# Kernel tuning notes

Hardware: AMD Instinct MI355X
Metric: run time of the kernel (lower is better)

Reference implementation:

```python
import jax, jax.numpy as jnp
import numpy as np

N = 1024
IN_F = 128
H0 = 192  # num_features * 2
H1 = 96   # num_features * 1
BN_EPS = 1e-5
SLOPE = 0.01  # LeakyReLU default negative slope


def setup_inputs() -> dict:
    key = jax.random.key(0)
    ks = jax.random.split(key, 8)
    node_feat = jax.random.normal(ks[0], (N, IN_F), dtype=jnp.float32)
    W0 = jax.random.normal(ks[1], (H0, IN_F), dtype=jnp.float32) * 0.05
    g0 = jnp.ones((H0,), jnp.float32); b0 = jnp.zeros((H0,), jnp.float32)
    m0 = jnp.zeros((H0,), jnp.float32); v0 = jnp.ones((H0,), jnp.float32)
    W1 = jax.random.normal(ks[2], (H1, H0), dtype=jnp.float32) * 0.05
    g1 = jnp.ones((H1,), jnp.float32); b1 = jnp.zeros((H1,), jnp.float32)
    m1 = jnp.zeros((H1,), jnp.float32); v1 = jnp.ones((H1,), jnp.float32)
    Wout = jax.random.normal(ks[3], (1, H1), dtype=jnp.float32) * 0.05
    bout = jnp.zeros((1,), jnp.float32)
    return dict(node_feat=node_feat, W0=W0, g0=g0, b0=b0, m0=m0, v0=v0,
                W1=W1, g1=g1, b1=b1, m1=m1, v1=v1, Wout=Wout, bout=bout)


def _bn(x, g, b, m, v):
    # BatchNorm2d in eval mode over channel axis (last axis here)
    return (x - m) * (g * jax.lax.rsqrt(v + BN_EPS)) + b


def _leaky(x):
    return jnp.where(x >= 0, x, SLOPE * x)


def reference(node_feat, W0, g0, b0, m0, v0, W1, g1, b1, m1, v1, Wout, bout):
    n = node_feat.shape[0]
    # pairwise abs diff: [N, N, F] (symmetric, so torch's i/j transpose is a no-op)
    x_ij = jnp.abs(node_feat[:, None, :] - node_feat[None, :, :])
    # 1x1 convs == per-(i,j) matmuls over channel axis
    h = _leaky(_bn(jnp.einsum('ijf,cf->ijc', x_ij, W0), g0, b0, m0, v0))
    h = _leaky(_bn(jnp.einsum('ijc,dc->ijd', h, W1), g1, b1, m1, v1))
    logits = jnp.einsum('ijd,od->ijo', h, Wout)[..., 0] + bout[0]  # [N, N]
    sim_val = jax.nn.sigmoid(logits)
    edge = sim_val + jnp.eye(n, dtype=sim_val.dtype) + 1e-6
    # torch sums over dim=1 of [1, N, N] -> normalize over the row index i
    edge = edge / jnp.sum(edge, axis=0, keepdims=True)
    return edge[None], sim_val  # edge_feat [1, N, N], sim_val [N, N]
```

## Files before the change

kernel.cpp:

```cpp
#include <hip/hip_runtime.h>
#include <hip/hip_bf16.h>
#include <math.h>

typedef float v4f __attribute__((ext_vector_type(4)));
typedef __bf16 bf16x8 __attribute__((ext_vector_type(8)));
typedef __bf16 bf16x4 __attribute__((ext_vector_type(4)));

#define NN   1024
#define INF  128
#define H0C  192
#define H1C  96

#define WS_W0BF   0
#define WS_W1BF   49152
#define WS_BN0SW  86016
#define WS_BN1SW  86784
#define WS_WOUTSW 87168
#define WS_PART   91648

__global__ __launch_bounds__(256) void prep_kernel(
    const float* __restrict__ W0, const float* __restrict__ g0,
    const float* __restrict__ b0, const float* __restrict__ m0,
    const float* __restrict__ v0, const float* __restrict__ W1,
    const float* __restrict__ g1, const float* __restrict__ b1,
    const float* __restrict__ m1, const float* __restrict__ v1,
    const float* __restrict__ Wout, char* __restrict__ ws)
{
    int e = blockIdx.x * 256 + threadIdx.x;
    __bf16* w0bf = (__bf16*)(ws + WS_W0BF);
    __bf16* w1bf = (__bf16*)(ws + WS_W1BF);
    float* bn0sw = (float*)(ws + WS_BN0SW);
    float* bn1sw = (float*)(ws + WS_BN1SW);
    float* woutsw = (float*)(ws + WS_WOUTSW);
    if (e < 24576) {
        int j = e & 7, lane = (e >> 3) & 63, t = e >> 9;
        int ks = t & 3, mt = t >> 2;
        int c = mt * 16 + (lane & 15);
        int k = ks * 32 + ((lane >> 4) << 3) + j;
        float s = g0[c] * rsqrtf(v0[c] + 1e-5f);
        w0bf[e] = (__bf16)(W0[c * INF + k] * s);
    } else if (e < 43008) {
        int e2 = e - 24576;
        int j = e2 & 7, lane = (e2 >> 3) & 63, t = e2 >> 9;
        int ks = t % 6, mt = t / 6;
        int c = mt * 16 + (lane & 15);
        int k = ks * 32 + ((lane >> 4) << 3) + j;
        float s = g1[c] * rsqrtf(v1[c] + 1e-5f);
        w1bf[e2] = (__bf16)(W1[c * H0C + k] * s);
    } else if (e < 43200) {
        int e3 = e - 43008;
        int q = e3 / 48, rem = e3 % 48, cm = rem >> 2, r = rem & 3;
        int c = cm * 16 + q * 4 + r;
        float s = g0[c] * rsqrtf(v0[c] + 1e-5f);
        bn0sw[e3] = b0[c] - m0[c] * s;
    } else if (e < 43296) {
        int e4 = e - 43200;
        int q = e4 / 24, rem = e4 % 24, mt = rem >> 2, r = rem & 3;
        int c = mt * 16 + q * 4 + r;
        float s = g1[c] * rsqrtf(v1[c] + 1e-5f);
        bn1sw[e4] = b1[c] - m1[c] * s;
    } else if (e < 43392) {
        int e5 = e - 43296;
        int q = e5 / 24, rem = e5 % 24, mt = rem >> 2, r = rem & 3;
        woutsw[e5] = Wout[mt * 16 + q * 4 + r];
    }
}

__global__ __launch_bounds__(256, 3) void edgenet_main(
    const float* __restrict__ feat, const char* __restrict__ ws,
    const float* __restrict__ boutp, float* __restrict__ sim_out)
{
    __shared__ __align__(16) char smem[51200];
    const int tid = threadIdx.x;
    const int lane = tid & 63;
    const int wave = tid >> 6;
    const int l16 = lane & 15;
    const int quad = lane >> 4;

    const int id = blockIdx.x;
    int bi = (int)((129.0f - sqrtf(16641.0f - 4.0f * (float)id)) * 0.5f);
    while (bi > 0 && bi * (129 - bi) > id) --bi;
    while ((bi + 1) * (128 - bi) <= id) ++bi;
    const int bj = 2 * bi + (id - bi * (129 - bi));
    const int i0 = bi << 4;
    const int j0 = bj << 3;
    const int jb = j0 + wave * 2;

    #pragma unroll
    for (int it = 0; it < 8; ++it) {
        int c = it * 256 + tid;
        int p = c >> 4;
        int f0 = (c & 15) << 3;
        int ii = p & 15, jj = p >> 4;
        const float* fi = feat + (i0 + ii) * INF + f0;
        const float* fj = feat + (j0 + jj) * INF + f0;
        float4 a0 = *(const float4*)fi;
        float4 a1 = *(const float4*)(fi + 4);
        float4 q0 = *(const float4*)fj;
        float4 q1 = *(const float4*)(fj + 4);
        bf16x8 x;
        x[0] = (__bf16)fabsf(a0.x - q0.x);
        x[1] = (__bf16)fabsf(a0.y - q0.y);
        x[2] = (__bf16)fabsf(a0.z - q0.z);
        x[3] = (__bf16)fabsf(a0.w - q0.w);
        x[4] = (__bf16)fabsf(a1.x - q1.x);
        x[5] = (__bf16)fabsf(a1.y - q1.y);
        x[6] = (__bf16)fabsf(a1.z - q1.z);
        x[7] = (__bf16)fabsf(a1.w - q1.w);
        *(bf16x8*)(smem + p * 272 + f0 * 2) = x;
    }
    __syncthreads();

    const bf16x8* w0v = (const bf16x8*)(ws + WS_W0BF);
    const bf16x8* w1v = (const bf16x8*)(ws + WS_W1BF);
    const float* bn0sw = (const float*)(ws + WS_BN0SW);
    const float* bn1sw = (const float*)(ws + WS_BN1SW);

    v4f acc1[3][8];
    #pragma unroll
    for (int mt = 0; mt < 3; ++mt) {
        v4f bb = *(const v4f*)(bn0sw + (quad * 12 + wave * 3 + mt) * 4);
        #pragma unroll
        for (int nt = 0; nt < 8; ++nt)
            acc1[mt][nt] = bb;
    }
    #pragma unroll
    for (int ks = 0; ks < 4; ++ks) {
        bf16x8 xk[8];
        #pragma unroll
        for (int nt = 0; nt < 8; ++nt)
            xk[nt] = *(const bf16x8*)(smem + (nt * 16 + l16) * 272 + ks * 64 + quad * 16);
        #pragma unroll
        for (int mt = 0; mt < 3; ++mt) {
            bf16x8 w = w0v[((wave * 3 + mt) * 4 + ks) * 64 + lane];
            #pragma unroll
            for (int nt = 0; nt < 8; ++nt)
                acc1[mt][nt] = __builtin_amdgcn_mfma_f32_16x16x32_bf16(
                    w, xk[nt], acc1[mt][nt], 0, 0, 0);
        }
    }
    __syncthreads();

    #pragma unroll
    for (int mt = 0; mt < 3; ++mt) {
        int chb = (wave * 3 + mt) * 16 + quad * 4;
        #pragma unroll
        for (int nt = 0; nt < 8; ++nt) {
            bf16x4 pk;
            #pragma unroll
            for (int r = 0; r < 4; ++r) {
                float v = acc1[mt][nt][r];
                v = fmaxf(v, 0.01f * v);
                pk[r] = (__bf16)v;
            }
            *(bf16x4*)(smem + (nt * 16 + l16) * 400 + chb * 2) = pk;
        }
    }
    __syncthreads();

    v4f acc2[6][2];
    #pragma unroll
    for (int mt = 0; mt < 6; ++mt) {
        v4f bb = *(const v4f*)(bn1sw + (quad * 6 + mt) * 4);
        acc2[mt][0] = bb;
        acc2[mt][1] = bb;
    }
    #pragma unroll
    for (int ks = 0; ks < 6; ++ks) {
        bf16x8 h0, h1;
        h0 = *(const bf16x8*)(smem + ((2 * wave + 0) * 16 + l16) * 400 + ks * 64 + quad * 16);
        h1 = *(const bf16x8*)(smem + ((2 * wave + 1) * 16 + l16) * 400 + ks * 64 + quad * 16);
        #pragma unroll
        for (int mt = 0; mt < 6; ++mt) {
            bf16x8 w = w1v[(mt * 6 + ks) * 64 + lane];
            acc2[mt][0] = __builtin_amdgcn_mfma_f32_16x16x32_bf16(w, h0, acc2[mt][0], 0, 0, 0);
            acc2[mt][1] = __builtin_amdgcn_mfma_f32_16x16x32_bf16(w, h1, acc2[mt][1], 0, 0, 0);
        }
    }

    const float* woutsw = (const float*)(ws + WS_WOUTSW);
    float part[2] = {0.f, 0.f};
    #pragma unroll
    for (int mt = 0; mt < 6; ++mt) {
        v4f wo = *(const v4f*)(woutsw + (quad * 6 + mt) * 4);
        #pragma unroll
        for (int t = 0; t < 2; ++t)
            #pragma unroll
            for (int r = 0; r < 4; ++r) {
                float v = acc2[mt][t][r];
                v = fmaxf(v, 0.01f * v);
                part[t] = fmaf(v, wo[r], part[t]);
            }
    }
    #pragma unroll
    for (int t = 0; t < 2; ++t) {
        part[t] += __shfl_xor(part[t], 16, 64);
        part[t] += __shfl_xor(part[t], 32, 64);
    }
    float z = (quad & 1) ? part[1] : part[0];
    float sv = 1.f / (1.f + expf(-(z + boutp[0])));
    if (quad < 2)
        sim_out[(i0 + l16) * NN + jb + (quad & 1)] = sv;
    else
        sim_out[(jb + (quad & 1)) * NN + i0 + l16] = sv;
}

__global__ __launch_bounds__(256) void colsum_kernel(
    const float* __restrict__ sim, float* __restrict__ part)
{
    __shared__ float red[4][64];
    int jl = threadIdx.x & 63;
    int ig = threadIdx.x >> 6;
    int j = blockIdx.x * 64 + jl;
    int ibase = blockIdx.y * 64 + ig * 16;
    float s = 0.f;
    #pragma unroll
    for (int r = 0; r < 16; ++r)
        s += sim[(ibase + r) * NN + j];
    red[ig][jl] = s;
    __syncthreads();
    if (ig == 0) {
        float t = red[0][jl] + red[1][jl] + red[2][jl] + red[3][jl];
        part[blockIdx.y * NN + j] = t;
    }
}

__global__ __launch_bounds__(256) void edge_kernel(
    const float* __restrict__ partsum, const float* __restrict__ sim,
    float* __restrict__ edge)
{
    int i = blockIdx.x;
    int jc = threadIdx.x << 2;
    float4 t = {0.f, 0.f, 0.f, 0.f};
    #pragma unroll
    for (int p = 0; p < 16; ++p) {
        float4 q = *(const float4*)(partsum + p * NN + jc);
        t.x += q.x; t.y += q.y; t.z += q.z; t.w += q.w;
    }
    const float cadd = 1.0f + (float)NN * 1e-6f;
    float4 s = *(const float4*)(sim + i * NN + jc);
    float4 o;
    o.x = (s.x + (i == jc + 0 ? 1.f : 0.f) + 1e-6f) / (t.x + cadd);
    o.y = (s.y + (i == jc + 1 ? 1.f : 0.f) + 1e-6f) / (t.y + cadd);
    o.z = (s.z + (i == jc + 2 ? 1.f : 0.f) + 1e-6f) / (t.z + cadd);
    o.w = (s.w + (i == jc + 3 ? 1.f : 0.f) + 1e-6f) / (t.w + cadd);
    *(float4*)(edge + i * NN + jc) = o;
}

extern "C" void kernel_launch(void* const* d_in, const int* in_sizes, int n_in,
                              void* d_out, int out_size, void* d_ws, size_t ws_size,
                              hipStream_t stream)
{
    const float* feat = (const float*)d_in[0];
    const float* W0   = (const float*)d_in[1];
    const float* g0   = (const float*)d_in[2];
    const float* b0   = (const float*)d_in[3];
    const float* m0   = (const float*)d_in[4];
    const float* v0   = (const float*)d_in[5];
    const float* W1   = (const float*)d_in[6];
    const float* g1   = (const float*)d_in[7];
    const float* b1   = (const float*)d_in[8];
    const float* m1   = (const float*)d_in[9];
    const float* v1   = (const float*)d_in[10];
    const float* Wout = (const float*)d_in[11];
    const float* bout = (const float*)d_in[12];
    char* ws = (char*)d_ws;
    float* edge = (float*)d_out;
    float* sim  = edge + NN * NN;
    float* part = (float*)(ws + WS_PART);

    prep_kernel<<<dim3(170), dim3(256), 0, stream>>>(
        W0, g0, b0, m0, v0, W1, g1, b1, m1, v1, Wout, ws);
    edgenet_main<<<dim3(4160), dim3(256), 0, stream>>>(feat, ws, bout, sim);
    colsum_kernel<<<dim3(16, 16), dim3(256), 0, stream>>>(sim, part);
    edge_kernel<<<dim3(1024), dim3(256), 0, stream>>>(part, sim, edge);
}
```

Before: 154.1 us.

## Fuse all stages into one persistent cooperative kernel with grid syncs

Replaces the four kernel launches (weight prep, main MLP, column sum, normalization) with a single cooperative persistent kernel that loops over tile ids and separates phases with grid-wide syncs. The column sum now produces reciprocal normalizers directly, so the final pass multiplies instead of divides. The pairwise-diff staging also reuses each i-row's feature loads across the 8 j rows. This removes launch gaps and the partial-sum buffer, at the cost of grid-sync overhead, a grid size capped at 704 persistent blocks, and an occupancy query on every call.

```diff
diff --git a/kernel.cpp b/kernel.cpp
--- a/kernel.cpp
+++ b/kernel.cpp
@@ -1,6 +1,9 @@
 #include <hip/hip_runtime.h>
+#include <hip/hip_cooperative_groups.h>
 #include <hip/hip_bf16.h>
 #include <math.h>
+
+namespace cg = cooperative_groups;
 
 typedef float v4f __attribute__((ext_vector_type(4)));
 typedef __bf16 bf16x8 __attribute__((ext_vector_type(8)));
@@ -16,59 +19,18 @@
 #define WS_BN0SW  86016
 #define WS_BN1SW  86784
 #define WS_WOUTSW 87168
-#define WS_PART   91648
-
-__global__ __launch_bounds__(256) void prep_kernel(
+#define WS_CINV   87552
+
+__global__ __launch_bounds__(256, 3) void edgenet_all(
+    const float* __restrict__ feat,
     const float* __restrict__ W0, const float* __restrict__ g0,
     const float* __restrict__ b0, const float* __restrict__ m0,
     const float* __restrict__ v0, const float* __restrict__ W1,
     const float* __restrict__ g1, const float* __restrict__ b1,
     const float* __restrict__ m1, const float* __restrict__ v1,
-    const float* __restrict__ Wout, char* __restrict__ ws)
-{
-    int e = blockIdx.x * 256 + threadIdx.x;
-    __bf16* w0bf = (__bf16*)(ws + WS_W0BF);
-    __bf16* w1bf = (__bf16*)(ws + WS_W1BF);
-    float* bn0sw = (float*)(ws + WS_BN0SW);
-    float* bn1sw = (float*)(ws + WS_BN1SW);
-    float* woutsw = (float*)(ws + WS_WOUTSW);
-    if (e < 24576) {
-        int j = e & 7, lane = (e >> 3) & 63, t = e >> 9;
-        int ks = t & 3, mt = t >> 2;
-        int c = mt * 16 + (lane & 15);
-        int k = ks * 32 + ((lane >> 4) << 3) + j;
-        float s = g0[c] * rsqrtf(v0[c] + 1e-5f);
-        w0bf[e] = (__bf16)(W0[c * INF + k] * s);
-    } else if (e < 43008) {
-        int e2 = e - 24576;
-        int j = e2 & 7, lane = (e2 >> 3) & 63, t = e2 >> 9;
-        int ks = t % 6, mt = t / 6;
-        int c = mt * 16 + (lane & 15);
-        int k = ks * 32 + ((lane >> 4) << 3) + j;
-        float s = g1[c] * rsqrtf(v1[c] + 1e-5f);
-        w1bf[e2] = (__bf16)(W1[c * H0C + k] * s);
-    } else if (e < 43200) {
-        int e3 = e - 43008;
-        int q = e3 / 48, rem = e3 % 48, cm = rem >> 2, r = rem & 3;
-        int c = cm * 16 + q * 4 + r;
-        float s = g0[c] * rsqrtf(v0[c] + 1e-5f);
-        bn0sw[e3] = b0[c] - m0[c] * s;
-    } else if (e < 43296) {
-        int e4 = e - 43200;
-        int q = e4 / 24, rem = e4 % 24, mt = rem >> 2, r = rem & 3;
-        int c = mt * 16 + q * 4 + r;
-        float s = g1[c] * rsqrtf(v1[c] + 1e-5f);
-        bn1sw[e4] = b1[c] - m1[c] * s;
-    } else if (e < 43392) {
-        int e5 = e - 43296;
-        int q = e5 / 24, rem = e5 % 24, mt = rem >> 2, r = rem & 3;
-        woutsw[e5] = Wout[mt * 16 + q * 4 + r];
-    }
-}
-
-__global__ __launch_bounds__(256, 3) void edgenet_main(
-    const float* __restrict__ feat, const char* __restrict__ ws,
-    const float* __restrict__ boutp, float* __restrict__ sim_out)
+    const float* __restrict__ Wout, const float* __restrict__ boutp,
+    char* __restrict__ ws, float* __restrict__ sim_out,
+    float* __restrict__ edge)
 {
     __shared__ __align__(16) char smem[51200];
     const int tid = threadIdx.x;
@@ -76,175 +38,227 @@
     const int wave = tid >> 6;
     const int l16 = lane & 15;
     const int quad = lane >> 4;
-
-    const int id = blockIdx.x;
-    int bi = (int)((129.0f - sqrtf(16641.0f - 4.0f * (float)id)) * 0.5f);
-    while (bi > 0 && bi * (129 - bi) > id) --bi;
-    while ((bi + 1) * (128 - bi) <= id) ++bi;
-    const int bj = 2 * bi + (id - bi * (129 - bi));
-    const int i0 = bi << 4;
-    const int j0 = bj << 3;
-    const int jb = j0 + wave * 2;
-
-    #pragma unroll
-    for (int it = 0; it < 8; ++it) {
-        int c = it * 256 + tid;
-        int p = c >> 4;
-        int f0 = (c & 15) << 3;
-        int ii = p & 15, jj = p >> 4;
-        const float* fi = feat + (i0 + ii) * INF + f0;
-        const float* fj = feat + (j0 + jj) * INF + f0;
-        float4 a0 = *(const float4*)fi;
-        float4 a1 = *(const float4*)(fi + 4);
-        float4 q0 = *(const float4*)fj;
-        float4 q1 = *(const float4*)(fj + 4);
-        bf16x8 x;
-        x[0] = (__bf16)fabsf(a0.x - q0.x);
-        x[1] = (__bf16)fabsf(a0.y - q0.y);
-        x[2] = (__bf16)fabsf(a0.z - q0.z);
-        x[3] = (__bf16)fabsf(a0.w - q0.w);
-        x[4] = (__bf16)fabsf(a1.x - q1.x);
-        x[5] = (__bf16)fabsf(a1.y - q1.y);
-        x[6] = (__bf16)fabsf(a1.z - q1.z);
-        x[7] = (__bf16)fabsf(a1.w - q1.w);
-        *(bf16x8*)(smem + p * 272 + f0 * 2) = x;
+    cg::grid_group grid = cg::this_grid();
+
+    {
+        int e = blockIdx.x * 256 + tid;
+        __bf16* w0bf = (__bf16*)(ws + WS_W0BF);
+        __bf16* w1bf = (__bf16*)(ws + WS_W1BF);
+        float* bn0sw = (float*)(ws + WS_BN0SW);
+        float* bn1sw = (float*)(ws + WS_BN1SW);
+        float* woutsw = (float*)(ws + WS_WOUTSW);
+        if (e < 24576) {
+            int j = e & 7, ln = (e >> 3) & 63, t = e >> 9;
+            int ks = t & 3, mt = t >> 2;
+            int c = mt * 16 + (ln & 15);
+            int k = ks * 32 + ((ln >> 4) << 3) + j;
+            float s = g0[c] * rsqrtf(v0[c] + 1e-5f);
+            w0bf[e] = (__bf16)(W0[c * INF + k] * s);
+        } else if (e < 43008) {
+            int e2 = e - 24576;
+            int j = e2 & 7, ln = (e2 >> 3) & 63, t = e2 >> 9;
+            int ks = t % 6, mt = t / 6;
+            int c = mt * 16 + (ln & 15);
+            int k = ks * 32 + ((ln >> 4) << 3) + j;
+            float s = g1[c] * rsqrtf(v1[c] + 1e-5f);
+            w1bf[e2] = (__bf16)(W1[c * H0C + k] * s);
+        } else if (e < 43200) {
+            int e3 = e - 43008;
+            int q = e3 / 48, rem = e3 % 48, cm = rem >> 2, r = rem & 3;
+            int c = cm * 16 + q * 4 + r;
+            float s = g0[c] * rsqrtf(v0[c] + 1e-5f);
+            bn0sw[e3] = b0[c] - m0[c] * s;
+        } else if (e < 43296) {
+            int e4 = e - 43200;
+            int q = e4 / 24, rem = e4 % 24, mt = rem >> 2, r = rem & 3;
+            int c = mt * 16 + q * 4 + r;
+            float s = g1[c] * rsqrtf(v1[c] + 1e-5f);
+            bn1sw[e4] = b1[c] - m1[c] * s;
+        } else if (e < 43392) {
+            int e5 = e - 43296;
+            int q = e5 / 24, rem = e5 % 24, mt = rem >> 2, r = rem & 3;
+            woutsw[e5] = Wout[mt * 16 + q * 4 + r];
+        }
     }
-    __syncthreads();
+    grid.sync();
 
     const bf16x8* w0v = (const bf16x8*)(ws + WS_W0BF);
     const bf16x8* w1v = (const bf16x8*)(ws + WS_W1BF);
     const float* bn0sw = (const float*)(ws + WS_BN0SW);
     const float* bn1sw = (const float*)(ws + WS_BN1SW);
-
-    v4f acc1[3][8];
-    #pragma unroll
-    for (int mt = 0; mt < 3; ++mt) {
-        v4f bb = *(const v4f*)(bn0sw + (quad * 12 + wave * 3 + mt) * 4);
-        #pragma unroll
-        for (int nt = 0; nt < 8; ++nt)
-            acc1[mt][nt] = bb;
+    const float* woutsw = (const float*)(ws + WS_WOUTSW);
+    const float bout0 = boutp[0];
+
+    for (int id = blockIdx.x; id < 4160; id += gridDim.x) {
+        __syncthreads();
+
+        int bi = (int)((129.0f - sqrtf(16641.0f - 4.0f * (float)id)) * 0.5f);
+        while (bi > 0 && bi * (129 - bi) > id) --bi;
+        while ((bi + 1) * (128 - bi) <= id) ++bi;
+        const int bj = 2 * bi + (id - bi * (129 - bi));
+        const int i0 = bi << 4;
+        const int j0 = bj << 3;
+        const int jb = j0 + wave * 2;
+
+        {
+            int ii = tid & 15, fblk = tid >> 4;
+            const float* fi = feat + (i0 + ii) * INF + fblk * 8;
+            float4 a0 = *(const float4*)fi;
+            float4 a1 = *(const float4*)(fi + 4);
+            const float* fj = feat + j0 * INF + fblk * 8;
+            char* sp = smem + ii * 272 + fblk * 16;
+            #pragma unroll
+            for (int jj = 0; jj < 8; ++jj) {
+                float4 q0 = *(const float4*)fj;
+                float4 q1 = *(const float4*)(fj + 4);
+                bf16x8 x;
+                x[0] = (__bf16)fabsf(a0.x - q0.x);
+                x[1] = (__bf16)fabsf(a0.y - q0.y);
+                x[2] = (__bf16)fabsf(a0.z - q0.z);
+                x[3] = (__bf16)fabsf(a0.w - q0.w);
+                x[4] = (__bf16)fabsf(a1.x - q1.x);
+                x[5] = (__bf16)fabsf(a1.y - q1.y);
+                x[6] = (__bf16)fabsf(a1.z - q1.z);
+                x[7] = (__bf16)fabsf(a1.w - q1.w);
+                *(bf16x8*)sp = x;
+                fj += INF;
+                sp += 16 * 272;
+            }
+        }
+        __syncthreads();
+
+        v4f acc1[3][8];
+        #pragma unroll
+        for (int mt = 0; mt < 3; ++mt) {
+            v4f bb = *(const v4f*)(bn0sw + (quad * 12 + wave * 3 + mt) * 4);
+            #pragma unroll
+            for (int nt = 0; nt < 8; ++nt)
+                acc1[mt][nt] = bb;
+        }
+        #pragma unroll
+        for (int ks = 0; ks < 4; ++ks) {
+            bf16x8 xk[8];
+            #pragma unroll
+            for (int nt = 0; nt < 8; ++nt)
+                xk[nt] = *(const bf16x8*)(smem + (nt * 16 + l16) * 272 + ks * 64 + quad * 16);
+            #pragma unroll
+            for (int mt = 0; mt < 3; ++mt) {
+                bf16x8 w = w0v[((wave * 3 + mt) * 4 + ks) * 64 + lane];
+                #pragma unroll
+                for (int nt = 0; nt < 8; ++nt)
+                    acc1[mt][nt] = __builtin_amdgcn_mfma_f32_16x16x32_bf16(
+                        w, xk[nt], acc1[mt][nt], 0, 0, 0);
+            }
+        }
+        __syncthreads();
+
+        #pragma unroll
+        for (int mt = 0; mt < 3; ++mt) {
+            int chb = (wave * 3 + mt) * 16 + quad * 4;
+            #pragma unroll
+            for (int nt = 0; nt < 8; ++nt) {
+                bf16x4 pk;
+                #pragma unroll
+                for (int r = 0; r < 4; ++r) {
+                    float v = acc1[mt][nt][r];
+                    v = fmaxf(v, 0.01f * v);
+                    pk[r] = (__bf16)v;
+                }
+                *(bf16x4*)(smem + (nt * 16 + l16) * 400 + chb * 2) = pk;
+            }
+        }
+        __syncthreads();
+
+        v4f acc2[6][2];
+        #pragma unroll
+        for (int mt = 0; mt < 6; ++mt) {
+            v4f bb = *(const v4f*)(bn1sw + (quad * 6 + mt) * 4);
+            acc2[mt][0] = bb;
+            acc2[mt][1] = bb;
+        }
+        #pragma unroll
+        for (int ks = 0; ks < 6; ++ks) {
+            bf16x8 h0 = *(const bf16x8*)(smem + ((2 * wave + 0) * 16 + l16) * 400 + ks * 64 + quad * 16);
+            bf16x8 h1 = *(const bf16x8*)(smem + ((2 * wave + 1) * 16 + l16) * 400 + ks * 64 + quad * 16);
+            #pragma unroll
+            for (int mt = 0; mt < 6; ++mt) {
+                bf16x8 w = w1v[(mt * 6 + ks) * 64 + lane];
+                acc2[mt][0] = __builtin_amdgcn_mfma_f32_16x16x32_bf16(w, h0, acc2[mt][0], 0, 0, 0);
+                acc2[mt][1] = __builtin_amdgcn_mfma_f32_16x16x32_bf16(w, h1, acc2[mt][1], 0, 0, 0);
+            }
+        }
+
+        float part[2] = {0.f, 0.f};
+        #pragma unroll
+        for (int mt = 0; mt < 6; ++mt) {
+            v4f wo = *(const v4f*)(woutsw + (quad * 6 + mt) * 4);
+            #pragma unroll
+            for (int t = 0; t < 2; ++t)
+                #pragma unroll
+                for (int r = 0; r < 4; ++r) {
+                    float v = acc2[mt][t][r];
+                    v = fmaxf(v, 0.01f * v);
+                    part[t] = fmaf(v, wo[r], part[t]);
+                }
+        }
+        #pragma unroll
+        for (int t = 0; t < 2; ++t) {
+            part[t] += __shfl_xor(part[t], 16, 64);
+            part[t] += __shfl_xor(part[t], 32, 64);
+        }
+        float z = (quad & 1) ? part[1] : part[0];
+        float sv = 1.f / (1.f + expf(-(z + bout0)));
+        if (quad < 2)
+            sim_out[(i0 + l16) * NN + jb + (quad & 1)] = sv;
+        else
+            sim_out[(jb + (quad & 1)) * NN + i0 + l16] = sv;
     }
-    #pragma unroll
-    for (int ks = 0; ks < 4; ++ks) {
-        bf16x8 xk[8];
-        #pragma unroll
-        for (int nt = 0; nt < 8; ++nt)
-            xk[nt] = *(const bf16x8*)(smem + (nt * 16 + l16) * 272 + ks * 64 + quad * 16);
-        #pragma unroll
-        for (int mt = 0; mt < 3; ++mt) {
-            bf16x8 w = w0v[((wave * 3 + mt) * 4 + ks) * 64 + lane];
-            #pragma unroll
-            for (int nt = 0; nt < 8; ++nt)
-                acc1[mt][nt] = __builtin_amdgcn_mfma_f32_16x16x32_bf16(
-                    w, xk[nt], acc1[mt][nt], 0, 0, 0);
+    grid.sync();
+
+    if (blockIdx.x < 256) {
+        int j0c = blockIdx.x * 4;
+        float4 a = {0.f, 0.f, 0.f, 0.f};
+        for (int r = tid; r < NN; r += 256) {
+            float4 s = *(const float4*)(sim_out + r * NN + j0c);
+            a.x += s.x; a.y += s.y; a.z += s.z; a.w += s.w;
+        }
+        #pragma unroll
+        for (int off = 1; off < 64; off <<= 1) {
+            a.x += __shfl_xor(a.x, off, 64);
+            a.y += __shfl_xor(a.y, off, 64);
+            a.z += __shfl_xor(a.z, off, 64);
+            a.w += __shfl_xor(a.w, off, 64);
+        }
+        float4* red = (float4*)smem;
+        if (lane == 0) red[wave] = a;
+        __syncthreads();
+        if (tid == 0) {
+            float4 t0 = red[0], t1 = red[1], t2 = red[2], t3 = red[3];
+            const float cadd = 1.0f + (float)NN * 1e-6f;
+            float4 ci;
+            ci.x = 1.0f / (t0.x + t1.x + t2.x + t3.x + cadd);
+            ci.y = 1.0f / (t0.y + t1.y + t2.y + t3.y + cadd);
+            ci.z = 1.0f / (t0.z + t1.z + t2.z + t3.z + cadd);
+            ci.w = 1.0f / (t0.w + t1.w + t2.w + t3.w + cadd);
+            *(float4*)((float*)(ws + WS_CINV) + j0c) = ci;
         }
     }
-    __syncthreads();
-
-    #pragma unroll
-    for (int mt = 0; mt < 3; ++mt) {
-        int chb = (wave * 3 + mt) * 16 + quad * 4;
-        #pragma unroll
-        for (int nt = 0; nt < 8; ++nt) {
-            bf16x4 pk;
-            #pragma unroll
-            for (int r = 0; r < 4; ++r) {
-                float v = acc1[mt][nt][r];
-                v = fmaxf(v, 0.01f * v);
-                pk[r] = (__bf16)v;
-            }
-            *(bf16x4*)(smem + (nt * 16 + l16) * 400 + chb * 2) = pk;
+    grid.sync();
+
+    {
+        const float* cinv = (const float*)(ws + WS_CINV);
+        int jc = tid << 2;
+        float4 w = *(const float4*)(cinv + jc);
+        for (int i = blockIdx.x; i < NN; i += gridDim.x) {
+            float4 s = *(const float4*)(sim_out + i * NN + jc);
+            float4 o;
+            o.x = (s.x + (i == jc + 0 ? 1.f : 0.f) + 1e-6f) * w.x;
+            o.y = (s.y + (i == jc + 1 ? 1.f : 0.f) + 1e-6f) * w.y;
+            o.z = (s.z + (i == jc + 2 ? 1.f : 0.f) + 1e-6f) * w.z;
+            o.w = (s.w + (i == jc + 3 ? 1.f : 0.f) + 1e-6f) * w.w;
+            *(float4*)(edge + i * NN + jc) = o;
         }
     }
-    __syncthreads();
-
-    v4f acc2[6][2];
-    #pragma unroll
-    for (int mt = 0; mt < 6; ++mt) {
-        v4f bb = *(const v4f*)(bn1sw + (quad * 6 + mt) * 4);
-        acc2[mt][0] = bb;
-        acc2[mt][1] = bb;
-    }
-    #pragma unroll
-    for (int ks = 0; ks < 6; ++ks) {
-        bf16x8 h0, h1;
-        h0 = *(const bf16x8*)(smem + ((2 * wave + 0) * 16 + l16) * 400 + ks * 64 + quad * 16);
-        h1 = *(const bf16x8*)(smem + ((2 * wave + 1) * 16 + l16) * 400 + ks * 64 + quad * 16);
-        #pragma unroll
-        for (int mt = 0; mt < 6; ++mt) {
-            bf16x8 w = w1v[(mt * 6 + ks) * 64 + lane];
-            acc2[mt][0] = __builtin_amdgcn_mfma_f32_16x16x32_bf16(w, h0, acc2[mt][0], 0, 0, 0);
-            acc2[mt][1] = __builtin_amdgcn_mfma_f32_16x16x32_bf16(w, h1, acc2[mt][1], 0, 0, 0);
-        }
-    }
-
-    const float* woutsw = (const float*)(ws + WS_WOUTSW);
-    float part[2] = {0.f, 0.f};
-    #pragma unroll
-    for (int mt = 0; mt < 6; ++mt) {
-        v4f wo = *(const v4f*)(woutsw + (quad * 6 + mt) * 4);
-        #pragma unroll
-        for (int t = 0; t < 2; ++t)
-            #pragma unroll
-            for (int r = 0; r < 4; ++r) {
-                float v = acc2[mt][t][r];
-                v = fmaxf(v, 0.01f * v);
-                part[t] = fmaf(v, wo[r], part[t]);
-            }
-    }
-    #pragma unroll
-    for (int t = 0; t < 2; ++t) {
-        part[t] += __shfl_xor(part[t], 16, 64);
-        part[t] += __shfl_xor(part[t], 32, 64);
-    }
-    float z = (quad & 1) ? part[1] : part[0];
-    float sv = 1.f / (1.f + expf(-(z + boutp[0])));
-    if (quad < 2)
-        sim_out[(i0 + l16) * NN + jb + (quad & 1)] = sv;
-    else
-        sim_out[(jb + (quad & 1)) * NN + i0 + l16] = sv;
-}
-
-__global__ __launch_bounds__(256) void colsum_kernel(
-    const float* __restrict__ sim, float* __restrict__ part)
-{
-    __shared__ float red[4][64];
-    int jl = threadIdx.x & 63;
-    int ig = threadIdx.x >> 6;
-    int j = blockIdx.x * 64 + jl;
-    int ibase = blockIdx.y * 64 + ig * 16;
-    float s = 0.f;
-    #pragma unroll
-    for (int r = 0; r < 16; ++r)
-        s += sim[(ibase + r) * NN + j];
-    red[ig][jl] = s;
-    __syncthreads();
-    if (ig == 0) {
-        float t = red[0][jl] + red[1][jl] + red[2][jl] + red[3][jl];
-        part[blockIdx.y * NN + j] = t;
-    }
-}
-
-__global__ __launch_bounds__(256) void edge_kernel(
-    const float* __restrict__ partsum, const float* __restrict__ sim,
-    float* __restrict__ edge)
-{
-    int i = blockIdx.x;
-    int jc = threadIdx.x << 2;
-    float4 t = {0.f, 0.f, 0.f, 0.f};
-    #pragma unroll
-    for (int p = 0; p < 16; ++p) {
-        float4 q = *(const float4*)(partsum + p * NN + jc);
-        t.x += q.x; t.y += q.y; t.z += q.z; t.w += q.w;
-    }
-    const float cadd = 1.0f + (float)NN * 1e-6f;
-    float4 s = *(const float4*)(sim + i * NN + jc);
-    float4 o;
-    o.x = (s.x + (i == jc + 0 ? 1.f : 0.f) + 1e-6f) / (t.x + cadd);
-    o.y = (s.y + (i == jc + 1 ? 1.f : 0.f) + 1e-6f) / (t.y + cadd);
-    o.z = (s.z + (i == jc + 2 ? 1.f : 0.f) + 1e-6f) / (t.z + cadd);
-    o.w = (s.w + (i == jc + 3 ? 1.f : 0.f) + 1e-6f) / (t.w + cadd);
-    *(float4*)(edge + i * NN + jc) = o;
 }
 
 extern "C" void kernel_launch(void* const* d_in, const int* in_sizes, int n_in,
@@ -267,11 +281,20 @@
     char* ws = (char*)d_ws;
     float* edge = (float*)d_out;
     float* sim  = edge + NN * NN;
-    float* part = (float*)(ws + WS_PART);
-
-    prep_kernel<<<dim3(170), dim3(256), 0, stream>>>(
-        W0, g0, b0, m0, v0, W1, g1, b1, m1, v1, Wout, ws);
-    edgenet_main<<<dim3(4160), dim3(256), 0, stream>>>(feat, ws, bout, sim);
-    colsum_kernel<<<dim3(16, 16), dim3(256), 0, stream>>>(sim, part);
-    edge_kernel<<<dim3(1024), dim3(256), 0, stream>>>(part, sim, edge);
+
+    int occ = 0;
+    (void)hipOccupancyMaxActiveBlocksPerMultiprocessor(&occ, edgenet_all, 256, 0);
+    if (occ < 1) occ = 1;
+    int maxg = occ * 256;
+    int gridsz = maxg < 704 ? maxg : 704;
+    if (gridsz < 256) gridsz = 256;
+
+    void* args[] = {
+        (void*)&feat, (void*)&W0, (void*)&g0, (void*)&b0, (void*)&m0,
+        (void*)&v0, (void*)&W1, (void*)&g1, (void*)&b1, (void*)&m1,
+        (void*)&v1, (void*)&Wout, (void*)&bout, (void*)&ws, (void*)&sim,
+        (void*)&edge
+    };
+    hipLaunchCooperativeKernel((void*)edgenet_all, dim3(gridsz), dim3(256),
+                               args, 0, stream);
 }
```

New measurement: 571.4 us. +270.8%, slower.

## Use sim symmetry for column sums via row reductions and precompute reciprocals

Applied to the files above, without the earlier changes.

Column sums of the symmetric sim matrix are now computed as row sums, one wave per row with coalesced float4 loads and shuffle reductions. The result is stored directly as a reciprocal, so the edge kernel does one multiply instead of reading 16 partial sums and dividing. The main kernel's pairwise-difference staging is also restructured so each thread loads its i-row features once and reuses them across 8 j rows. The row-sum path relies on sim being exactly symmetric, which the kernel guarantees because it writes both triangles from the same value. It launches only 64 blocks, which may leave much of the GPU idle.

```diff
diff --git a/kernel.cpp b/kernel.cpp
--- a/kernel.cpp
+++ b/kernel.cpp
@@ -16,7 +16,7 @@
 #define WS_BN0SW  86016
 #define WS_BN1SW  86784
 #define WS_WOUTSW 87168
-#define WS_PART   91648
+#define WS_CINV   87552
 
 __global__ __launch_bounds__(256) void prep_kernel(
     const float* __restrict__ W0, const float* __restrict__ g0,
@@ -86,28 +86,30 @@
     const int j0 = bj << 3;
     const int jb = j0 + wave * 2;
 
-    #pragma unroll
-    for (int it = 0; it < 8; ++it) {
-        int c = it * 256 + tid;
-        int p = c >> 4;
-        int f0 = (c & 15) << 3;
-        int ii = p & 15, jj = p >> 4;
-        const float* fi = feat + (i0 + ii) * INF + f0;
-        const float* fj = feat + (j0 + jj) * INF + f0;
+    {
+        int ii = tid & 15, fblk = tid >> 4;
+        const float* fi = feat + (i0 + ii) * INF + fblk * 8;
         float4 a0 = *(const float4*)fi;
         float4 a1 = *(const float4*)(fi + 4);
-        float4 q0 = *(const float4*)fj;
-        float4 q1 = *(const float4*)(fj + 4);
-        bf16x8 x;
-        x[0] = (__bf16)fabsf(a0.x - q0.x);
-        x[1] = (__bf16)fabsf(a0.y - q0.y);
-        x[2] = (__bf16)fabsf(a0.z - q0.z);
-        x[3] = (__bf16)fabsf(a0.w - q0.w);
-        x[4] = (__bf16)fabsf(a1.x - q1.x);
-        x[5] = (__bf16)fabsf(a1.y - q1.y);
-        x[6] = (__bf16)fabsf(a1.z - q1.z);
-        x[7] = (__bf16)fabsf(a1.w - q1.w);
-        *(bf16x8*)(smem + p * 272 + f0 * 2) = x;
+        const float* fj = feat + j0 * INF + fblk * 8;
+        char* sp = smem + ii * 272 + fblk * 16;
+        #pragma unroll
+        for (int jj = 0; jj < 8; ++jj) {
+            float4 q0 = *(const float4*)fj;
+            float4 q1 = *(const float4*)(fj + 4);
+            bf16x8 x;
+            x[0] = (__bf16)fabsf(a0.x - q0.x);
+            x[1] = (__bf16)fabsf(a0.y - q0.y);
+            x[2] = (__bf16)fabsf(a0.z - q0.z);
+            x[3] = (__bf16)fabsf(a0.w - q0.w);
+            x[4] = (__bf16)fabsf(a1.x - q1.x);
+            x[5] = (__bf16)fabsf(a1.y - q1.y);
+            x[6] = (__bf16)fabsf(a1.z - q1.z);
+            x[7] = (__bf16)fabsf(a1.w - q1.w);
+            *(bf16x8*)sp = x;
+            fj += INF;
+            sp += 16 * 272;
+        }
     }
     __syncthreads();
 
@@ -167,9 +169,8 @@
     }
     #pragma unroll
     for (int ks = 0; ks < 6; ++ks) {
-        bf16x8 h0, h1;
-        h0 = *(const bf16x8*)(smem + ((2 * wave + 0) * 16 + l16) * 400 + ks * 64 + quad * 16);
-        h1 = *(const bf16x8*)(smem + ((2 * wave + 1) * 16 + l16) * 400 + ks * 64 + quad * 16);
+        bf16x8 h0 = *(const bf16x8*)(smem + ((2 * wave + 0) * 16 + l16) * 400 + ks * 64 + quad * 16);
+        bf16x8 h1 = *(const bf16x8*)(smem + ((2 * wave + 1) * 16 + l16) * 400 + ks * 64 + quad * 16);
         #pragma unroll
         for (int mt = 0; mt < 6; ++mt) {
             bf16x8 w = w1v[(mt * 6 + ks) * 64 + lane];
@@ -205,45 +206,43 @@
         sim_out[(jb + (quad & 1)) * NN + i0 + l16] = sv;
 }
 
-__global__ __launch_bounds__(256) void colsum_kernel(
-    const float* __restrict__ sim, float* __restrict__ part)
-{
-    __shared__ float red[4][64];
-    int jl = threadIdx.x & 63;
-    int ig = threadIdx.x >> 6;
-    int j = blockIdx.x * 64 + jl;
-    int ibase = blockIdx.y * 64 + ig * 16;
-    float s = 0.f;
-    #pragma unroll
-    for (int r = 0; r < 16; ++r)
-        s += sim[(ibase + r) * NN + j];
-    red[ig][jl] = s;
-    __syncthreads();
-    if (ig == 0) {
-        float t = red[0][jl] + red[1][jl] + red[2][jl] + red[3][jl];
-        part[blockIdx.y * NN + j] = t;
+__global__ __launch_bounds__(256) void cinv_kernel(
+    const float* __restrict__ sim, float* __restrict__ cinv)
+{
+    const int lane = threadIdx.x & 63;
+    const int wave = threadIdx.x >> 6;
+    const float cadd = 1.0f + (float)NN * 1e-6f;
+    #pragma unroll
+    for (int rr = 0; rr < 4; ++rr) {
+        int j = blockIdx.x * 16 + wave * 4 + rr;
+        const float4* row = (const float4*)(sim + j * NN);
+        float4 a0 = row[lane];
+        float4 a1 = row[lane + 64];
+        float4 a2 = row[lane + 128];
+        float4 a3 = row[lane + 192];
+        float s = (a0.x + a0.y + a0.z + a0.w) + (a1.x + a1.y + a1.z + a1.w)
+                + (a2.x + a2.y + a2.z + a2.w) + (a3.x + a3.y + a3.z + a3.w);
+        #pragma unroll
+        for (int off = 1; off < 64; off <<= 1)
+            s += __shfl_xor(s, off, 64);
+        if (lane == 0)
+            cinv[j] = 1.0f / (s + cadd);
     }
 }
 
 __global__ __launch_bounds__(256) void edge_kernel(
-    const float* __restrict__ partsum, const float* __restrict__ sim,
+    const float* __restrict__ cinv, const float* __restrict__ sim,
     float* __restrict__ edge)
 {
     int i = blockIdx.x;
     int jc = threadIdx.x << 2;
-    float4 t = {0.f, 0.f, 0.f, 0.f};
-    #pragma unroll
-    for (int p = 0; p < 16; ++p) {
-        float4 q = *(const float4*)(partsum + p * NN + jc);
-        t.x += q.x; t.y += q.y; t.z += q.z; t.w += q.w;
-    }
-    const float cadd = 1.0f + (float)NN * 1e-6f;
+    float4 w = *(const float4*)(cinv + jc);
     float4 s = *(const float4*)(sim + i * NN + jc);
     float4 o;
-    o.x = (s.x + (i == jc + 0 ? 1.f : 0.f) + 1e-6f) / (t.x + cadd);
-    o.y = (s.y + (i == jc + 1 ? 1.f : 0.f) + 1e-6f) / (t.y + cadd);
-    o.z = (s.z + (i == jc + 2 ? 1.f : 0.f) + 1e-6f) / (t.z + cadd);
-    o.w = (s.w + (i == jc + 3 ? 1.f : 0.f) + 1e-6f) / (t.w + cadd);
+    o.x = (s.x + (i == jc + 0 ? 1.f : 0.f) + 1e-6f) * w.x;
+    o.y = (s.y + (i == jc + 1 ? 1.f : 0.f) + 1e-6f) * w.y;
+    o.z = (s.z + (i == jc + 2 ? 1.f : 0.f) + 1e-6f) * w.z;
+    o.w = (s.w + (i == jc + 3 ? 1.f : 0.f) + 1e-6f) * w.w;
     *(float4*)(edge + i * NN + jc) = o;
 }
 
@@ -267,11 +266,11 @@
     char* ws = (char*)d_ws;
     float* edge = (float*)d_out;
     float* sim  = edge + NN * NN;
-    float* part = (float*)(ws + WS_PART);
+    float* cinv = (float*)(ws + WS_CINV);
 
     prep_kernel<<<dim3(170), dim3(256), 0, stream>>>(
         W0, g0, b0, m0, v0, W1, g1, b1, m1, v1, Wout, ws);
     edgenet_main<<<dim3(4160), dim3(256), 0, stream>>>(feat, ws, bout, sim);
-    colsum_kernel<<<dim3(16, 16), dim3(256), 0, stream>>>(sim, part);
-    edge_kernel<<<dim3(1024), dim3(256), 0, stream>>>(part, sim, edge);
-}
+    cinv_kernel<<<dim3(64), dim3(256), 0, stream>>>(sim, cinv);
+    edge_kernel<<<dim3(1024), dim3(256), 0, stream>>>(cinv, sim, edge);
+}
```

Result: no change. 155.7 us (+1.1%).
